# Optimization experiments

Hardware: AMD Instinct MI355X
Metric: run time of the kernel (lower is better)

Reference implementation:

```python
import jax, jax.numpy as jnp
import numpy as np
import math

B, N, C, EV, H = 16, 4096, 256, 64, 8
A_, B_, C_ = 10, 10, 10  # query group sizes a, b, c
TEMP = 0.1


def setup_inputs() -> dict:
    key = jax.random.key(0)
    ks = jax.random.split(key, 24)
    x = jax.random.normal(ks[0], (B, N, C), jnp.float32)
    origin_x = jax.random.normal(ks[1], (B, N, C), jnp.float32)
    evectors = jax.random.normal(ks[2], (B, A_ + B_ + C_, EV), jnp.float32)
    # numv: cumulative node counts; per-graph diff with 3*diff <= N
    diffs = jax.random.randint(ks[3], (B,), 64, N // 3 + 1)
    numv = jnp.concatenate([jnp.zeros((1,), jnp.int32), jnp.cumsum(diffs).astype(jnp.int32)])
    # additive cross mask: valid where position < 3*diff
    pos = jnp.arange(N)
    valid = pos[None, :] < (3 * diffs)[:, None]  # [B, N]
    mask_cross = jnp.where(valid, 0.0, -1e9).astype(jnp.float32)[:, None, :] * jnp.ones((1, A_ + B_ + C_, 1), jnp.float32)
    s = 0.02
    p = lambda k, shp: jax.random.normal(k, shp, jnp.float32) * s
    inp = {
        'x': x, 'origin_x': origin_x, 'evectors': evectors,
        'mask_cross': mask_cross, 'numv': numv,
        'Wq_G': p(ks[4], (C, EV)), 'Wq_D': p(ks[5], (C, EV)), 'Wq_L': p(ks[6], (C, EV)),
        'Wk_G': p(ks[7], (C, C)), 'Wk_D': p(ks[8], (C, C)), 'Wk_L': p(ks[9], (C, C)),
        'Wv_G': p(ks[10], (C, C)), 'bv_G': jnp.zeros((C,), jnp.float32),
        'Wv_D': p(ks[11], (C, C)), 'bv_D': jnp.zeros((C,), jnp.float32),
        'Wv_L': p(ks[12], (C, C)), 'bv_L': jnp.zeros((C,), jnp.float32),
        'Wo': p(ks[13], (C, C)), 'bo': jnp.zeros((C,), jnp.float32),
    }
    return inp


def _forward(x, origin_x, evectors, mask_cross, numv,
             Wq_G, Wq_D, Wq_L, Wk_G, Wk_D, Wk_L,
             Wv_G, bv_G, Wv_D, bv_D, Wv_L, bv_L, Wo, bo):
    dv = C
    dh = dv // H
    nq = A_ + B_ + C_
    # --- query: per-group linear projections on evectors ---
    Q = jnp.concatenate([
        evectors[:, :A_] @ Wq_G.T,
        evectors[:, A_:A_ + B_] @ Wq_D.T,
        evectors[:, A_ + B_:nq] @ Wq_L.T,
    ], axis=1)  # [B, nq, dv]
    # --- ragged K/V construction: group by position vs per-graph diff ---
    diffs = (numv[1:] - numv[:-1]).astype(jnp.int32)  # [B]
    pos = jnp.arange(N)[None, :]  # [1, N]
    d = diffs[:, None]
    g0 = (pos < d).astype(x.dtype)[..., None]
    g1 = ((pos >= d) & (pos < 2 * d)).astype(x.dtype)[..., None]
    g2 = ((pos >= 2 * d) & (pos < 3 * d)).astype(x.dtype)[..., None]
    Kd = g0 * (x @ Wk_G.T) + g1 * (x @ Wk_D.T) + g2 * (x @ Wk_L.T)  # [B, N, dv]
    Vd = (g0 * (origin_x @ Wv_G.T + bv_G)
          + g1 * (origin_x @ Wv_D.T + bv_D)
          + g2 * (origin_x @ Wv_L.T + bv_L))  # [B, N, dv]
    # --- per-head weight decorrelation loss on Q ---
    Qh = Q.reshape(B, nq, H, dh).transpose(2, 0, 1, 3)  # [H, B, nq, dh]
    wd = jnp.asarray(0.0, Q.dtype)
    for lo, sz in ((0, A_), (A_, B_), (A_ + B_, C_)):
        if sz > 1:
            G = Qh[:, :, lo:lo + sz]  # [H, B, sz, dh]
            corr = jnp.einsum('hbik,hbjk->hbij', G, G)
            diff_m = corr - jnp.eye(sz, dtype=Q.dtype)
            fro = jnp.sqrt(jnp.sum(diff_m * diff_m, axis=(-2, -1)))  # [H, B]
            wd = wd + fro.mean(axis=1).sum()
    # --- masked, temperature-scaled multi-head attention ---
    Kh = Kd.reshape(B, N, H, dh)
    Vh = Vd.reshape(B, N, H, dh)
    Qh2 = Q.reshape(B, nq, H, dh)
    scores = jnp.einsum('bqhd,bkhd->bhqk', Qh2, Kh) / (math.sqrt(dv) * TEMP)
    scores = scores + mask_cross[:, None, :, :]
    Aw = jax.nn.softmax(scores, axis=-1)
    out = jnp.einsum('bhqk,bkhd->bqhd', Aw, Vh).reshape(B, nq, dv)
    out = out + jax.nn.relu(out @ Wo.T + bo)
    nrm = jnp.linalg.norm(out, axis=2, keepdims=True)
    out = out / jnp.maximum(nrm, 1e-12)
    return out, wd


def reference(x, origin_x, evectors, mask_cross, numv,
              Wq_G, Wq_D, Wq_L, Wk_G, Wk_D, Wk_L,
              Wv_G, bv_G, Wv_D, bv_D, Wv_L, bv_L, Wo, bo):
    return _forward(x, origin_x, evectors, mask_cross, numv,
                    Wq_G, Wq_D, Wq_L, Wk_G, Wk_D, Wk_L,
                    Wv_G, bv_G, Wv_D, bv_D, Wv_L, bv_L, Wo, bo)
```

## Files before the change

### kernel.cpp

```cpp
#include <hip/hip_runtime.h>
#include <math.h>


typedef __bf16 bf16x8 __attribute__((ext_vector_type(8)));
typedef float  f32x4  __attribute__((ext_vector_type(4)));

namespace {
constexpr int kB   = 16;
constexpr int kN   = 4096;
constexpr int kC   = 256;
constexpr int kEV  = 64;
constexpr int kH   = 8;
constexpr int kDH  = 32;
constexpr int kNQ  = 30;
constexpr int kCH  = 64;
constexpr int kMaxT = 1056;
constexpr int kGrid = 512;
constexpr float kScale = 0.625f;
}

__device__ __forceinline__ unsigned short f32_to_bf16(float f) {
  unsigned int u = __float_as_uint(f);
  unsigned int r = (u + 0x7FFFu + ((u >> 16) & 1u)) >> 16;
  return (unsigned short)r;
}
__device__ __forceinline__ unsigned int pack_bf16(float a, float b) {
  return (unsigned int)f32_to_bf16(a) | ((unsigned int)f32_to_bf16(b) << 16);
}
__device__ __forceinline__ f32x4 splat4(float v) {
  f32x4 r; r[0] = v; r[1] = v; r[2] = v; r[3] = v; return r;
}
__device__ __forceinline__ int swz_f(int row) {
  return ((row & 7) << 2) | (((row >> 3) & 1) << 1);
}

__global__ __launch_bounds__(256) void prep_kernel(
    const float* __restrict__ ev,
    const float* __restrict__ WqG, const float* __restrict__ WqD,
    const float* __restrict__ WqL,
    const float* __restrict__ WkG, const float* __restrict__ WkD,
    const float* __restrict__ WkL,
    const float* __restrict__ WvG, const float* __restrict__ WvD,
    const float* __restrict__ WvL,
    unsigned short* __restrict__ Wb,
    unsigned short* __restrict__ WkT,
    float* __restrict__ Qw, unsigned short* __restrict__ Qb,
    float* __restrict__ wdp)
{
  const int bid = blockIdx.x, tid = threadIdx.x;

  if (bid < 96) {
    const int mat = bid >> 5;
    const float* src = (mat == 0) ? WvG : (mat == 1) ? WvD : WvL;
    const int i0 = (((bid & 31) << 8) + tid) * 8;
    const float4* s4 = (const float4*)(src + i0);
    float4 a = s4[0], b = s4[1];
    uint4 pack = make_uint4(pack_bf16(a.x, a.y), pack_bf16(a.z, a.w),
                            pack_bf16(b.x, b.y), pack_bf16(b.z, b.w));
    *(uint4*)(Wb + (size_t)mat * 65536 + i0) = pack;
    return;
  }

  if (bid < 144) {
    __shared__ float ts[64][65];
    const int t2 = bid - 96;
    const int mat = t2 >> 4, tile = t2 & 15;
    const int r0 = (tile >> 2) * 64, c0 = (tile & 3) * 64;
    const float* src = (mat == 0) ? WkG : (mat == 1) ? WkD : WkL;
#pragma unroll
    for (int it = 0; it < 16; ++it) {
      const int idx = tid + it * 256;
      const int r = idx >> 6, c = idx & 63;
      ts[r][c] = src[(size_t)(r0 + r) * kC + c0 + c];
    }
    __syncthreads();
#pragma unroll
    for (int it = 0; it < 16; ++it) {
      const int idx = tid + it * 256;
      const int r = idx >> 6, c = idx & 63;
      WkT[(size_t)mat * 65536 + (size_t)(c0 + r) * kC + r0 + c] =
          f32_to_bf16(ts[c][r]);
    }
    return;
  }

  if (bid < 656) {
    __shared__ float e[kEV];
    const int idx = bid - 144;
    const int b = idx >> 5, qq = idx & 31;
    if (qq >= kNQ) { Qb[((size_t)(b * 32 + qq)) * kC + tid] = 0; return; }
    if (tid < kEV) e[tid] = ev[((size_t)(b * kNQ + qq)) * kEV + tid];
    __syncthreads();
    const float* W = (qq < 10) ? WqG : (qq < 20) ? WqD : WqL;
    const float4* wr = (const float4*)(W + (size_t)tid * kEV);
    const float4* er = (const float4*)e;
    float s = 0.0f;
#pragma unroll
    for (int j = 0; j < kEV / 4; ++j) {
      float4 w = wr[j], v = er[j];
      s = fmaf(v.x, w.x, s); s = fmaf(v.y, w.y, s);
      s = fmaf(v.z, w.z, s); s = fmaf(v.w, w.w, s);
    }
    Qw[((size_t)(b * kNQ + qq)) * kC + tid] = s;
    Qb[((size_t)(b * 32 + qq)) * kC + tid] = f32_to_bf16(s * kScale);
    return;
  }

  {
    __shared__ float evs[10][64];
    __shared__ float Qblk[10][33];
    __shared__ float sred[256];
    const int w = bid - 656;
    const int b = w / 24, r = w % 24, g = r >> 3, h = r & 7;
    const int lo = g * 10;
    const float* Wqg = (g == 0) ? WqG : (g == 1) ? WqD : WqL;
    for (int i = tid; i < 640; i += 256) {
      const int q = i >> 6, e2 = i & 63;
      evs[q][e2] = ev[((size_t)(b * kNQ + lo + q)) * kEV + e2];
    }
    __syncthreads();
    for (int i = tid; i < 320; i += 256) {
      const int q = i >> 5, kk = i & 31;
      const float* wp = Wqg + (size_t)(h * 32 + kk) * kEV;
      float s = 0.0f;
#pragma unroll
      for (int e4 = 0; e4 < 16; ++e4) {
        float4 ev4 = *(const float4*)&evs[q][e4 * 4];
        float4 w4  = *(const float4*)(wp + e4 * 4);
        s = fmaf(ev4.x, w4.x, s); s = fmaf(ev4.y, w4.y, s);
        s = fmaf(ev4.z, w4.z, s); s = fmaf(ev4.w, w4.w, s);
      }
      Qblk[q][kk] = s;
    }
    __syncthreads();
    float v = 0.0f;
    if (tid < 100) {
      const int i = tid / 10, j = tid % 10;
      float corr = 0.0f;
#pragma unroll
      for (int k = 0; k < kDH; ++k) corr = fmaf(Qblk[i][k], Qblk[j][k], corr);
      const float diff = corr - (i == j ? 1.0f : 0.0f);
      v = diff * diff;
    }
    sred[tid] = v;
    __syncthreads();
    for (int s2 = 128; s2 > 0; s2 >>= 1) {
      if (tid < s2) sred[tid] += sred[tid + s2];
      __syncthreads();
    }
    if (tid == 0) wdp[w] = sqrtf(sred[0]) * (1.0f / 16.0f);
  }
}

__global__ __launch_bounds__(512) void wqk_kernel(
    const unsigned short* __restrict__ Qb,
    const unsigned short* __restrict__ WkT,
    unsigned short* __restrict__ Wqkb)
{
  const int bid = blockIdx.x, tid = threadIdx.x;
  const int b = bid / 3, g = bid % 3;
  const int lane = tid & 63, h = tid >> 6;
  const int lg = lane >> 4, lr = lane & 15;

  const unsigned short* WkT_g = WkT + (size_t)g * 65536;

  bf16x8 aq[2];
#pragma unroll
  for (int mt = 0; mt < 2; ++mt)
    aq[mt] = *reinterpret_cast<const bf16x8*>(
        Qb + (size_t)(b * 32 + mt * 16 + lr) * kC + h * 32 + lg * 8);

  f32x4 acc[2][16];
#pragma unroll
  for (int mt = 0; mt < 2; ++mt)
#pragma unroll
    for (int nt = 0; nt < 16; ++nt) acc[mt][nt] = splat4(0.0f);

#pragma unroll
  for (int nt = 0; nt < 16; ++nt) {
    bf16x8 bw = *reinterpret_cast<const bf16x8*>(
        WkT_g + (size_t)(nt * 16 + lr) * kC + h * 32 + lg * 8);
    acc[0][nt] = __builtin_amdgcn_mfma_f32_16x16x32_bf16(aq[0], bw, acc[0][nt], 0, 0, 0);
    acc[1][nt] = __builtin_amdgcn_mfma_f32_16x16x32_bf16(aq[1], bw, acc[1][nt], 0, 0, 0);
  }

  unsigned short* dst = Wqkb + ((size_t)((b * 3 + g) * 8 + h)) * 32 * kC;
#pragma unroll
  for (int mt = 0; mt < 2; ++mt)
#pragma unroll
    for (int nt = 0; nt < 16; ++nt)
#pragma unroll
      for (int j = 0; j < 4; ++j) {
        const int q = mt * 16 + lg * 4 + j;
        dst[(size_t)q * kC + nt * 16 + lr] = f32_to_bf16(acc[mt][nt][j]);
      }
}

__global__ __launch_bounds__(512, 4) void chunk_kernel(
    const float* __restrict__ x, const float* __restrict__ ox,
    const int* __restrict__ numv,
    const unsigned short* __restrict__ Wb,
    const float* __restrict__ bvG, const float* __restrict__ bvD,
    const float* __restrict__ bvL,
    const unsigned short* __restrict__ Wqkb,
    float* __restrict__ Pl, float* __restrict__ Po)
{
  __shared__ unsigned short Xs[kCH * kC];
  __shared__ unsigned short Ov[kCH * kC];

  const int tid = threadIdx.x;
  const int lane = tid & 63, wv = tid >> 6;
  const int lg = lane >> 4, lr = lane & 15;
  const int wcol0 = wv * 32;
  const int h = wv;

  int nv[17];
#pragma unroll
  for (int i = 0; i < 17; ++i) nv[i] = numv[i];
  int Tall = 0;
#pragma unroll
  for (int bb = 0; bb < kB; ++bb)
    Tall += 3 * ((nv[bb + 1] - nv[bb] + 63) >> 6);

  const int vp = (blockIdx.x & 7) * (kGrid / 8) + (blockIdx.x >> 3);
  const int lo = (vp * Tall) / kGrid;
  const int hi = ((vp + 1) * Tall) / kGrid;

  for (int tt = lo; tt < hi; ++tt) {
    int rem = tt, b = -1, g = 0, ch = 0;
#pragma unroll
    for (int bb = 0; bb < kB; ++bb) {
      const int cb = (nv[bb + 1] - nv[bb] + 63) >> 6;
#pragma unroll
      for (int gg = 0; gg < 3; ++gg) {
        if (b < 0) { if (rem < cb) { b = bb; g = gg; ch = rem; } else rem -= cb; }
      }
    }

    const int d = nv[b + 1] - nv[b];
    const int row0 = g * d + ch * kCH;
    const int nvalid = min(min(kCH, d - ch * kCH), kN - row0);

    const unsigned short* Wv_g = Wb + (size_t)g * 65536;
    const float* bv = (g == 0) ? bvG : (g == 1) ? bvD : bvL;
    const unsigned short* Wqk_h =
        Wqkb + ((size_t)((b * 3 + g) * 8 + h)) * 32 * kC;

    {
      const float* xb = x + (size_t)b * kN * kC;
      const float* ob = ox + (size_t)b * kN * kC;
      float4 xa[8], oa[8];
      int off[4];
#pragma unroll
      for (int i = 0; i < 4; ++i) {
        const int cid = tid + i * 512;
        const int row = cid >> 5, c5 = cid & 31;
        const int rg = min(row0 + row, kN - 1);
        off[i] = rg * kC + c5 * 8;
        const float4* sx = (const float4*)(xb + off[i]);
        xa[2 * i] = sx[0]; xa[2 * i + 1] = sx[1];
      }
#pragma unroll
      for (int i = 0; i < 4; ++i) {
        const float4* so = (const float4*)(ob + off[i]);
        oa[2 * i] = so[0]; oa[2 * i + 1] = so[1];
      }
#pragma unroll
      for (int i = 0; i < 4; ++i) {
        const int cid = tid + i * 512;
        const int row = cid >> 5, c5 = cid & 31;
        const int base = row * kC + ((c5 ^ swz_f(row)) * 8);
        *(uint4*)(Xs + base) = make_uint4(
            pack_bf16(xa[2 * i].x, xa[2 * i].y), pack_bf16(xa[2 * i].z, xa[2 * i].w),
            pack_bf16(xa[2 * i + 1].x, xa[2 * i + 1].y),
            pack_bf16(xa[2 * i + 1].z, xa[2 * i + 1].w));
        *(uint4*)(Ov + base) = make_uint4(
            pack_bf16(oa[2 * i].x, oa[2 * i].y), pack_bf16(oa[2 * i].z, oa[2 * i].w),
            pack_bf16(oa[2 * i + 1].x, oa[2 * i + 1].y),
            pack_bf16(oa[2 * i + 1].z, oa[2 * i + 1].w));
      }
    }
    __syncthreads();

    f32x4 s[4][2];
#pragma unroll
    for (int m = 0; m < 4; ++m)
#pragma unroll
      for (int n = 0; n < 2; ++n) s[m][n] = splat4(0.0f);

#pragma unroll
    for (int kt = 0; kt < 8; ++kt) {
      bf16x8 a[4];
#pragma unroll
      for (int m = 0; m < 4; ++m) {
        const int row = m * 16 + lr;
        const int c16 = (kt * 4 + lg) ^ swz_f(row);
        a[m] = *reinterpret_cast<const bf16x8*>(Xs + row * kC + c16 * 8);
      }
      const int k0 = kt * 32 + lg * 8;
#pragma unroll
      for (int n = 0; n < 2; ++n) {
        bf16x8 bq = *reinterpret_cast<const bf16x8*>(
            Wqk_h + (size_t)(n * 16 + lr) * kC + k0);
#pragma unroll
        for (int m = 0; m < 4; ++m)
          s[m][n] = __builtin_amdgcn_mfma_f32_16x16x32_bf16(a[m], bq, s[m][n], 0, 0, 0);
      }
    }

    unsigned int pp[4][2][2];
    f32x4 lsum[2];
    lsum[0] = splat4(0.0f); lsum[1] = splat4(0.0f);
#pragma unroll
    for (int m = 0; m < 4; ++m)
#pragma unroll
      for (int n = 0; n < 2; ++n) {
        f32x4 pv;
#pragma unroll
        for (int j = 0; j < 4; ++j) {
          const int key = m * 16 + lg * 4 + j;
          pv[j] = (key < nvalid) ? __expf(s[m][n][j]) : 0.0f;
        }
        lsum[n] += pv;
        pp[m][n][0] = pack_bf16(pv[0], pv[1]);
        pp[m][n][1] = pack_bf16(pv[2], pv[3]);
      }
    float ls[2];
#pragma unroll
    for (int n = 0; n < 2; ++n) {
      float v = (lsum[n][0] + lsum[n][1]) + (lsum[n][2] + lsum[n][3]);
      v += __shfl_xor(v, 16);
      v += __shfl_xor(v, 32);
      ls[n] = v;
    }
    if (lg == 0) {
#pragma unroll
      for (int n = 0; n < 2; ++n) {
        const int q = n * 16 + lr;
        if (q < kNQ) Pl[((size_t)tt * kNQ + q) * kH + h] = ls[n];
      }
    }

    f32x4 vacc[4][2];
#pragma unroll
    for (int n = 0; n < 2; ++n) {
      const float bvv = bv[wcol0 + n * 16 + lr];
#pragma unroll
      for (int m = 0; m < 4; ++m) vacc[m][n] = splat4(bvv);
    }
#pragma unroll
    for (int kt = 0; kt < 8; ++kt) {
      bf16x8 a[4];
#pragma unroll
      for (int m = 0; m < 4; ++m) {
        const int row = m * 16 + lr;
        const int c16 = (kt * 4 + lg) ^ swz_f(row);
        a[m] = *reinterpret_cast<const bf16x8*>(Ov + row * kC + c16 * 8);
      }
      const int k0 = kt * 32 + lg * 8;
#pragma unroll
      for (int n = 0; n < 2; ++n) {
        bf16x8 bw = *reinterpret_cast<const bf16x8*>(
            Wv_g + (size_t)(wcol0 + n * 16 + lr) * kC + k0);
#pragma unroll
        for (int m = 0; m < 4; ++m)
          vacc[m][n] = __builtin_amdgcn_mfma_f32_16x16x32_bf16(a[m], bw, vacc[m][n], 0, 0, 0);
      }
    }
    __syncthreads();

    unsigned short* Pw = Xs + wv * 2048;
#pragma unroll
    for (int m = 0; m < 4; ++m)
#pragma unroll
      for (int n = 0; n < 2; ++n) {
        const int q = n * 16 + lr;
        const int ckp = (2 * m + (lg >> 1)) ^ (q & 7);
        unsigned short* pa = Pw + q * kCH + ckp * 8 + (lg & 1) * 4;
        *(unsigned int*)(pa) = pp[m][n][0];
        *(unsigned int*)(pa + 2) = pp[m][n][1];
      }

#pragma unroll
    for (int m = 0; m < 4; ++m)
#pragma unroll
      for (int n = 0; n < 2; ++n) {
        const int col = wcol0 + n * 16 + lr;
        const int r0 = m * 16 + lg * 4;
        unsigned short us[4];
#pragma unroll
        for (int j = 0; j < 4; ++j) us[j] = f32_to_bf16(vacc[m][n][j]);
        const int ck = (r0 >> 3) ^ (col & 7);
        *(uint2*)(Ov + col * kCH + ck * 8 + (r0 & 7)) =
            make_uint2((unsigned int)us[0] | ((unsigned int)us[1] << 16),
                       (unsigned int)us[2] | ((unsigned int)us[3] << 16));
      }

    f32x4 o[2][2];
#pragma unroll
    for (int m = 0; m < 2; ++m)
#pragma unroll
      for (int n = 0; n < 2; ++n) o[m][n] = splat4(0.0f);

#pragma unroll
    for (int ks = 0; ks < 2; ++ks) {
      bf16x8 ap[2];
#pragma unroll
      for (int mq = 0; mq < 2; ++mq) {
        const int q = mq * 16 + lr;
        ap[mq] = *reinterpret_cast<const bf16x8*>(
            Pw + q * kCH + (((ks * 4 + lg) ^ (q & 7))) * 8);
      }
#pragma unroll
      for (int n = 0; n < 2; ++n) {
        const int col = wcol0 + n * 16 + lr;
        bf16x8 bvf = *reinterpret_cast<const bf16x8*>(
            Ov + col * kCH + (((ks * 4 + lg) ^ (col & 7))) * 8);
        o[0][n] = __builtin_amdgcn_mfma_f32_16x16x32_bf16(ap[0], bvf, o[0][n], 0, 0, 0);
        o[1][n] = __builtin_amdgcn_mfma_f32_16x16x32_bf16(ap[1], bvf, o[1][n], 0, 0, 0);
      }
    }

#pragma unroll
    for (int mq = 0; mq < 2; ++mq)
#pragma unroll
      for (int n = 0; n < 2; ++n)
#pragma unroll
        for (int j = 0; j < 4; ++j) {
          const int q = mq * 16 + lg * 4 + j;
          if (q < kNQ)
            Po[(((size_t)tt * kNQ + q) * kH + h) * kDH + n * 16 + lr] = o[mq][n][j];
        }

    if (tt + 1 < hi) __syncthreads();
  }
}

__global__ __launch_bounds__(256) void combine_kernel(
    const float* __restrict__ Pl, const float* __restrict__ Po,
    const int* __restrict__ numv,
    const float* __restrict__ Wo, const float* __restrict__ bo,
    const float* __restrict__ wdp,
    float* __restrict__ out)
{
  const int bq = blockIdx.x;
  const int tid = threadIdx.x;

  if (bq == kB * kNQ) {
    float v = wdp[tid] + ((tid < 128) ? wdp[tid + 256] : 0.0f);
#pragma unroll
    for (int off = 32; off > 0; off >>= 1) v += __shfl_down(v, off);
    __shared__ float red[4];
    if ((tid & 63) == 0) red[tid >> 6] = v;
    __syncthreads();
    if (tid == 0)
      out[(size_t)kB * kNQ * kC] = red[0] + red[1] + red[2] + red[3];
    return;
  }

  const int b = bq / kNQ, q = bq % kNQ;
  const int h = tid >> 5, kk = tid & 31;

  int base = 0, cnt = 0, S = 0;
#pragma unroll
  for (int bb = 0; bb < kB; ++bb) {
    const int c3 = 3 * ((numv[bb + 1] - numv[bb] + 63) >> 6);
    if (bb == b) { base = S; cnt = c3; }
    S += c3;
  }

  float l = 0.0f, oacc = 0.0f;
#pragma unroll 4
  for (int i = 0; i < cnt; ++i) {
    const size_t idx = ((size_t)(base + i) * kNQ + q) * kH + h;
    l += Pl[idx];
    oacc += Po[idx * kDH + kk];
  }
  const float attn = oacc / l;

  __shared__ float row[kC];
  row[tid] = attn;
  __syncthreads();

  const float4* wr = (const float4*)(Wo + (size_t)tid * kC);
  const float4* rr = (const float4*)row;
  float s = 0.0f;
#pragma unroll
  for (int j = 0; j < kC / 4; ++j) {
    float4 w = wr[j], v = rr[j];
    s = fmaf(v.x, w.x, s); s = fmaf(v.y, w.y, s);
    s = fmaf(v.z, w.z, s); s = fmaf(v.w, w.w, s);
  }
  s += bo[tid];
  const float y = attn + fmaxf(s, 0.0f);

  float v = y * y;
#pragma unroll
  for (int off = 32; off > 0; off >>= 1) v += __shfl_down(v, off);
  __shared__ float red[4];
  if ((tid & 63) == 0) red[tid >> 6] = v;
  __syncthreads();
  const float tot = red[0] + red[1] + red[2] + red[3];
  const float nrm = fmaxf(sqrtf(tot), 1e-12f);
  out[(size_t)bq * kC + tid] = y / nrm;
}

extern "C" void kernel_launch(void* const* d_in, const int* in_sizes, int n_in,
                              void* d_out, int out_size, void* d_ws, size_t ws_size,
                              hipStream_t stream) {
  const float* x    = (const float*)d_in[0];
  const float* ox   = (const float*)d_in[1];
  const float* ev   = (const float*)d_in[2];
  const int*   numv = (const int*)d_in[4];
  const float* WqG  = (const float*)d_in[5];
  const float* WqD  = (const float*)d_in[6];
  const float* WqL  = (const float*)d_in[7];
  const float* WkG  = (const float*)d_in[8];
  const float* WkD  = (const float*)d_in[9];
  const float* WkL  = (const float*)d_in[10];
  const float* WvG  = (const float*)d_in[11];
  const float* bvG  = (const float*)d_in[12];
  const float* WvD  = (const float*)d_in[13];
  const float* bvD  = (const float*)d_in[14];
  const float* WvL  = (const float*)d_in[15];
  const float* bvL  = (const float*)d_in[16];
  const float* Wo   = (const float*)d_in[17];
  const float* bo   = (const float*)d_in[18];

  float* out = (float*)d_out;
  char*  ws  = (char*)d_ws;

  size_t off = 0;
  float* Qw = (float*)(ws + off);                   off += 491520;
  unsigned short* Qb   = (unsigned short*)(ws + off); off += 262144;
  unsigned short* Wb   = (unsigned short*)(ws + off); off += 393216;
  unsigned short* WkT  = (unsigned short*)(ws + off); off += 393216;
  unsigned short* Wqkb = (unsigned short*)(ws + off); off += 6291456;
  float* Pl  = (float*)(ws + off);  off += (size_t)kMaxT * kNQ * kH * 4;
  float* Po  = (float*)(ws + off);  off += (size_t)kMaxT * kNQ * kH * kDH * 4;
  float* wdp = (float*)(ws + off);  off += 1536;

  prep_kernel<<<1040, 256, 0, stream>>>(ev, WqG, WqD, WqL,
                                        WkG, WkD, WkL, WvG, WvD, WvL,
                                        Wb, WkT, Qw, Qb, wdp);
  wqk_kernel<<<48, 512, 0, stream>>>(Qb, WkT, Wqkb);
  chunk_kernel<<<kGrid, 512, 0, stream>>>(
      x, ox, numv, Wb, bvG, bvD, bvL, Wqkb, Pl, Po);
  combine_kernel<<<kB * kNQ + 1, 256, 0, stream>>>(Pl, Po, numv, Wo, bo, wdp, out);
}
```

Baseline: 105.2 us.

## Halve attention chunk size, store partial outputs in bf16, double occupancy

Chunk size drops from 64 to 32 keys, which halves LDS and register use per block so the launch bound can ask for 8 blocks per CU instead of 4. The V tile is now stored per wave in LDS. Partial attention outputs are written as bf16 through LDS with vectorized stores, and the combine kernel reads them as bf16. This doubles the number of partial tiles the combine kernel must reduce and lowers the precision of the partial sums.

```diff
diff --git a/kernel.cpp b/kernel.cpp
--- a/kernel.cpp
+++ b/kernel.cpp
@@ -13,8 +13,8 @@
 constexpr int kH   = 8;
 constexpr int kDH  = 32;
 constexpr int kNQ  = 30;
-constexpr int kCH  = 64;
-constexpr int kMaxT = 1056;
+constexpr int kCH  = 32;
+constexpr int kMaxT = 2064;
 constexpr int kGrid = 512;
 constexpr float kScale = 0.625f;
 }
@@ -26,6 +26,9 @@
 }
 __device__ __forceinline__ unsigned int pack_bf16(float a, float b) {
   return (unsigned int)f32_to_bf16(a) | ((unsigned int)f32_to_bf16(b) << 16);
+}
+__device__ __forceinline__ float bf16_to_f32(unsigned short u) {
+  return __uint_as_float((unsigned int)u << 16);
 }
 __device__ __forceinline__ f32x4 splat4(float v) {
   f32x4 r; r[0] = v; r[1] = v; r[2] = v; r[3] = v; return r;
@@ -196,14 +199,14 @@
       }
 }
 
-__global__ __launch_bounds__(512, 4) void chunk_kernel(
+__global__ __launch_bounds__(512, 8) void chunk_kernel(
     const float* __restrict__ x, const float* __restrict__ ox,
     const int* __restrict__ numv,
     const unsigned short* __restrict__ Wb,
     const float* __restrict__ bvG, const float* __restrict__ bvD,
     const float* __restrict__ bvL,
     const unsigned short* __restrict__ Wqkb,
-    float* __restrict__ Pl, float* __restrict__ Po)
+    float* __restrict__ Pl, unsigned short* __restrict__ Po)
 {
   __shared__ unsigned short Xs[kCH * kC];
   __shared__ unsigned short Ov[kCH * kC];
@@ -220,7 +223,7 @@
   int Tall = 0;
 #pragma unroll
   for (int bb = 0; bb < kB; ++bb)
-    Tall += 3 * ((nv[bb + 1] - nv[bb] + 63) >> 6);
+    Tall += 3 * ((nv[bb + 1] - nv[bb] + kCH - 1) / kCH);
 
   const int vp = (blockIdx.x & 7) * (kGrid / 8) + (blockIdx.x >> 3);
   const int lo = (vp * Tall) / kGrid;
@@ -230,7 +233,7 @@
     int rem = tt, b = -1, g = 0, ch = 0;
 #pragma unroll
     for (int bb = 0; bb < kB; ++bb) {
-      const int cb = (nv[bb + 1] - nv[bb] + 63) >> 6;
+      const int cb = (nv[bb + 1] - nv[bb] + kCH - 1) / kCH;
 #pragma unroll
       for (int gg = 0; gg < 3; ++gg) {
         if (b < 0) { if (rem < cb) { b = bb; g = gg; ch = rem; } else rem -= cb; }
@@ -239,7 +242,7 @@
 
     const int d = nv[b + 1] - nv[b];
     const int row0 = g * d + ch * kCH;
-    const int nvalid = min(min(kCH, d - ch * kCH), kN - row0);
+    const int nvalid = min(kCH, d - ch * kCH);
 
     const unsigned short* Wv_g = Wb + (size_t)g * 65536;
     const float* bv = (g == 0) ? bvG : (g == 1) ? bvD : bvL;
@@ -249,26 +252,26 @@
     {
       const float* xb = x + (size_t)b * kN * kC;
       const float* ob = ox + (size_t)b * kN * kC;
-      float4 xa[8], oa[8];
-      int off[4];
-#pragma unroll
-      for (int i = 0; i < 4; ++i) {
-        const int cid = tid + i * 512;
-        const int row = cid >> 5, c5 = cid & 31;
+      float4 xa[4], oa[4];
+      int off[2];
+#pragma unroll
+      for (int i = 0; i < 2; ++i) {
+        const int sid = tid + i * 512;
+        const int row = sid >> 5, c5 = sid & 31;
         const int rg = min(row0 + row, kN - 1);
         off[i] = rg * kC + c5 * 8;
         const float4* sx = (const float4*)(xb + off[i]);
         xa[2 * i] = sx[0]; xa[2 * i + 1] = sx[1];
       }
 #pragma unroll
-      for (int i = 0; i < 4; ++i) {
+      for (int i = 0; i < 2; ++i) {
         const float4* so = (const float4*)(ob + off[i]);
         oa[2 * i] = so[0]; oa[2 * i + 1] = so[1];
       }
 #pragma unroll
-      for (int i = 0; i < 4; ++i) {
-        const int cid = tid + i * 512;
-        const int row = cid >> 5, c5 = cid & 31;
+      for (int i = 0; i < 2; ++i) {
+        const int sid = tid + i * 512;
+        const int row = sid >> 5, c5 = sid & 31;
         const int base = row * kC + ((c5 ^ swz_f(row)) * 8);
         *(uint4*)(Xs + base) = make_uint4(
             pack_bf16(xa[2 * i].x, xa[2 * i].y), pack_bf16(xa[2 * i].z, xa[2 * i].w),
@@ -282,17 +285,17 @@
     }
     __syncthreads();
 
-    f32x4 s[4][2];
-#pragma unroll
-    for (int m = 0; m < 4; ++m)
+    f32x4 s[2][2];
+#pragma unroll
+    for (int m = 0; m < 2; ++m)
 #pragma unroll
       for (int n = 0; n < 2; ++n) s[m][n] = splat4(0.0f);
 
 #pragma unroll
     for (int kt = 0; kt < 8; ++kt) {
-      bf16x8 a[4];
-#pragma unroll
-      for (int m = 0; m < 4; ++m) {
+      bf16x8 a[2];
+#pragma unroll
+      for (int m = 0; m < 2; ++m) {
         const int row = m * 16 + lr;
         const int c16 = (kt * 4 + lg) ^ swz_f(row);
         a[m] = *reinterpret_cast<const bf16x8*>(Xs + row * kC + c16 * 8);
@@ -303,16 +306,16 @@
         bf16x8 bq = *reinterpret_cast<const bf16x8*>(
             Wqk_h + (size_t)(n * 16 + lr) * kC + k0);
 #pragma unroll
-        for (int m = 0; m < 4; ++m)
+        for (int m = 0; m < 2; ++m)
           s[m][n] = __builtin_amdgcn_mfma_f32_16x16x32_bf16(a[m], bq, s[m][n], 0, 0, 0);
       }
     }
 
-    unsigned int pp[4][2][2];
+    unsigned int pp[2][2][2];
     f32x4 lsum[2];
     lsum[0] = splat4(0.0f); lsum[1] = splat4(0.0f);
 #pragma unroll
-    for (int m = 0; m < 4; ++m)
+    for (int m = 0; m < 2; ++m)
 #pragma unroll
       for (int n = 0; n < 2; ++n) {
         f32x4 pv;
@@ -341,18 +344,18 @@
       }
     }
 
-    f32x4 vacc[4][2];
+    f32x4 vacc[2][2];
 #pragma unroll
     for (int n = 0; n < 2; ++n) {
       const float bvv = bv[wcol0 + n * 16 + lr];
 #pragma unroll
-      for (int m = 0; m < 4; ++m) vacc[m][n] = splat4(bvv);
+      for (int m = 0; m < 2; ++m) vacc[m][n] = splat4(bvv);
     }
 #pragma unroll
     for (int kt = 0; kt < 8; ++kt) {
-      bf16x8 a[4];
-#pragma unroll
-      for (int m = 0; m < 4; ++m) {
+      bf16x8 a[2];
+#pragma unroll
+      for (int m = 0; m < 2; ++m) {
         const int row = m * 16 + lr;
         const int c16 = (kt * 4 + lg) ^ swz_f(row);
         a[m] = *reinterpret_cast<const bf16x8*>(Ov + row * kC + c16 * 8);
@@ -363,37 +366,37 @@
         bf16x8 bw = *reinterpret_cast<const bf16x8*>(
             Wv_g + (size_t)(wcol0 + n * 16 + lr) * kC + k0);
 #pragma unroll
-        for (int m = 0; m < 4; ++m)
+        for (int m = 0; m < 2; ++m)
           vacc[m][n] = __builtin_amdgcn_mfma_f32_16x16x32_bf16(a[m], bw, vacc[m][n], 0, 0, 0);
       }
     }
     __syncthreads();
 
-    unsigned short* Pw = Xs + wv * 2048;
-#pragma unroll
-    for (int m = 0; m < 4; ++m)
+    unsigned short* Pw = Xs + wv * 1024;
+#pragma unroll
+    for (int m = 0; m < 2; ++m)
 #pragma unroll
       for (int n = 0; n < 2; ++n) {
         const int q = n * 16 + lr;
-        const int ckp = (2 * m + (lg >> 1)) ^ (q & 7);
-        unsigned short* pa = Pw + q * kCH + ckp * 8 + (lg & 1) * 4;
+        const int ck = (2 * m + (lg >> 1)) ^ (q & 3);
+        unsigned short* pa = Pw + q * kCH + ck * 8 + (lg & 1) * 4;
         *(unsigned int*)(pa) = pp[m][n][0];
         *(unsigned int*)(pa + 2) = pp[m][n][1];
       }
 
-#pragma unroll
-    for (int m = 0; m < 4; ++m)
-#pragma unroll
-      for (int n = 0; n < 2; ++n) {
-        const int col = wcol0 + n * 16 + lr;
-        const int r0 = m * 16 + lg * 4;
-        unsigned short us[4];
-#pragma unroll
-        for (int j = 0; j < 4; ++j) us[j] = f32_to_bf16(vacc[m][n][j]);
-        const int ck = (r0 >> 3) ^ (col & 7);
-        *(uint2*)(Ov + col * kCH + ck * 8 + (r0 & 7)) =
-            make_uint2((unsigned int)us[0] | ((unsigned int)us[1] << 16),
-                       (unsigned int)us[2] | ((unsigned int)us[3] << 16));
+    unsigned short* Vw = Ov + wv * 1024;
+#pragma unroll
+    for (int m = 0; m < 2; ++m)
+#pragma unroll
+      for (int n = 0; n < 2; ++n) {
+        const int cl = n * 16 + lr;
+        const int k0r = m * 16 + lg * 4;
+        const int ck = (2 * m + (lg >> 1)) ^ (cl & 3);
+        *(unsigned int*)(Vw + cl * kCH + ck * 8 + (lg & 1) * 4) =
+            pack_bf16(vacc[m][n][0], vacc[m][n][1]);
+        *(unsigned int*)(Vw + cl * kCH + ck * 8 + (lg & 1) * 4 + 2) =
+            pack_bf16(vacc[m][n][2], vacc[m][n][3]);
+        (void)k0r;
       }
 
     f32x4 o[2][2];
@@ -402,20 +405,19 @@
 #pragma unroll
       for (int n = 0; n < 2; ++n) o[m][n] = splat4(0.0f);
 
-#pragma unroll
-    for (int ks = 0; ks < 2; ++ks) {
+    {
       bf16x8 ap[2];
 #pragma unroll
       for (int mq = 0; mq < 2; ++mq) {
         const int q = mq * 16 + lr;
         ap[mq] = *reinterpret_cast<const bf16x8*>(
-            Pw + q * kCH + (((ks * 4 + lg) ^ (q & 7))) * 8);
-      }
-#pragma unroll
-      for (int n = 0; n < 2; ++n) {
-        const int col = wcol0 + n * 16 + lr;
+            Pw + q * kCH + ((lg ^ (q & 3))) * 8);
+      }
+#pragma unroll
+      for (int n = 0; n < 2; ++n) {
+        const int cl = n * 16 + lr;
         bf16x8 bvf = *reinterpret_cast<const bf16x8*>(
-            Ov + col * kCH + (((ks * 4 + lg) ^ (col & 7))) * 8);
+            Vw + cl * kCH + ((lg ^ (cl & 3))) * 8);
         o[0][n] = __builtin_amdgcn_mfma_f32_16x16x32_bf16(ap[0], bvf, o[0][n], 0, 0, 0);
         o[1][n] = __builtin_amdgcn_mfma_f32_16x16x32_bf16(ap[1], bvf, o[1][n], 0, 0, 0);
       }
@@ -428,16 +430,24 @@
 #pragma unroll
         for (int j = 0; j < 4; ++j) {
           const int q = mq * 16 + lg * 4 + j;
-          if (q < kNQ)
-            Po[(((size_t)tt * kNQ + q) * kH + h) * kDH + n * 16 + lr] = o[mq][n][j];
+          Pw[q * kDH + n * 16 + lr] = f32_to_bf16(o[mq][n][j]);
         }
+    {
+      unsigned short* pdst = Po + (((size_t)tt * kNQ) * kH + h) * kDH;
+#pragma unroll 2
+      for (int idx = lane; idx < kNQ * 4; idx += 64) {
+        const int q = idx >> 2, c = idx & 3;
+        uint4 v4 = *(const uint4*)(Pw + q * kDH + c * 8);
+        *(uint4*)(pdst + (size_t)q * kH * kDH + c * 8) = v4;
+      }
+    }
 
     if (tt + 1 < hi) __syncthreads();
   }
 }
 
 __global__ __launch_bounds__(256) void combine_kernel(
-    const float* __restrict__ Pl, const float* __restrict__ Po,
+    const float* __restrict__ Pl, const unsigned short* __restrict__ Po,
     const int* __restrict__ numv,
     const float* __restrict__ Wo, const float* __restrict__ bo,
     const float* __restrict__ wdp,
@@ -464,7 +474,7 @@
   int base = 0, cnt = 0, S = 0;
 #pragma unroll
   for (int bb = 0; bb < kB; ++bb) {
-    const int c3 = 3 * ((numv[bb + 1] - numv[bb] + 63) >> 6);
+    const int c3 = 3 * ((numv[bb + 1] - numv[bb] + kCH - 1) / kCH);
     if (bb == b) { base = S; cnt = c3; }
     S += c3;
   }
@@ -474,7 +484,7 @@
   for (int i = 0; i < cnt; ++i) {
     const size_t idx = ((size_t)(base + i) * kNQ + q) * kH + h;
     l += Pl[idx];
-    oacc += Po[idx * kDH + kk];
+    oacc += bf16_to_f32(Po[idx * kDH + kk]);
   }
   const float attn = oacc / l;
 
@@ -536,9 +546,10 @@
   unsigned short* Wb   = (unsigned short*)(ws + off); off += 393216;
   unsigned short* WkT  = (unsigned short*)(ws + off); off += 393216;
   unsigned short* Wqkb = (unsigned short*)(ws + off); off += 6291456;
-  float* Pl  = (float*)(ws + off);  off += (size_t)kMaxT * kNQ * kH * 4;
-  float* Po  = (float*)(ws + off);  off += (size_t)kMaxT * kNQ * kH * kDH * 4;
-  float* wdp = (float*)(ws + off);  off += 1536;
+  float* Pl = (float*)(ws + off);           off += (size_t)kMaxT * kNQ * kH * 4;
+  unsigned short* Po = (unsigned short*)(ws + off);
+  off += (size_t)kMaxT * kNQ * kH * kDH * 2;
+  float* wdp = (float*)(ws + off);          off += 1536;
 
   prep_kernel<<<1040, 256, 0, stream>>>(ev, WqG, WqD, WqL,
                                         WkG, WkD, WkL, WvG, WvD, WvL,
```

New measurement: 153.7 us. 46.1% more time.

## Prefetch next chunk's inputs into registers and store partial outputs as bf16

Applied to the files above, without the earlier changes.

The chunk kernel now loads the next chunk's x/origin_x rows into registers right after the LDS barrier, so the global loads overlap the current chunk's MFMA work. The grid is halved to 256 and the occupancy hint drops to 2 blocks per CU to make room for the extra live registers. Partial attention outputs are staged in LDS and written as bf16 in a head-major layout with coalesced 16-byte stores, which halves Po traffic for the combine kernel at some precision cost. Plain __syncthreads are replaced by a barrier that waits only on LDS counters.

```diff
diff --git a/kernel.cpp b/kernel.cpp
--- a/kernel.cpp
+++ b/kernel.cpp
@@ -15,9 +15,15 @@
 constexpr int kNQ  = 30;
 constexpr int kCH  = 64;
 constexpr int kMaxT = 1056;
-constexpr int kGrid = 512;
+constexpr int kGrid = 256;
 constexpr float kScale = 0.625f;
 }
+
+#define BAR_LDS() do {                                        \
+    asm volatile("s_waitcnt lgkmcnt(0)" ::: "memory");        \
+    __builtin_amdgcn_s_barrier();                             \
+    __builtin_amdgcn_sched_barrier(0);                        \
+  } while (0)
 
 __device__ __forceinline__ unsigned short f32_to_bf16(float f) {
   unsigned int u = __float_as_uint(f);
@@ -26,6 +32,9 @@
 }
 __device__ __forceinline__ unsigned int pack_bf16(float a, float b) {
   return (unsigned int)f32_to_bf16(a) | ((unsigned int)f32_to_bf16(b) << 16);
+}
+__device__ __forceinline__ float bf16_to_f32(unsigned short u) {
+  return __uint_as_float((unsigned int)u << 16);
 }
 __device__ __forceinline__ f32x4 splat4(float v) {
   f32x4 r; r[0] = v; r[1] = v; r[2] = v; r[3] = v; return r;
@@ -196,14 +205,14 @@
       }
 }
 
-__global__ __launch_bounds__(512, 4) void chunk_kernel(
+__global__ __launch_bounds__(512, 2) void chunk_kernel(
     const float* __restrict__ x, const float* __restrict__ ox,
     const int* __restrict__ numv,
     const unsigned short* __restrict__ Wb,
     const float* __restrict__ bvG, const float* __restrict__ bvD,
     const float* __restrict__ bvL,
     const unsigned short* __restrict__ Wqkb,
-    float* __restrict__ Pl, float* __restrict__ Po)
+    float* __restrict__ Pl, unsigned short* __restrict__ Po)
 {
   __shared__ unsigned short Xs[kCH * kC];
   __shared__ unsigned short Ov[kCH * kC];
@@ -220,23 +229,50 @@
   int Tall = 0;
 #pragma unroll
   for (int bb = 0; bb < kB; ++bb)
-    Tall += 3 * ((nv[bb + 1] - nv[bb] + 63) >> 6);
+    Tall += 3 * ((nv[bb + 1] - nv[bb] + kCH - 1) / kCH);
 
   const int vp = (blockIdx.x & 7) * (kGrid / 8) + (blockIdx.x >> 3);
   const int lo = (vp * Tall) / kGrid;
   const int hi = ((vp + 1) * Tall) / kGrid;
-
-  for (int tt = lo; tt < hi; ++tt) {
-    int rem = tt, b = -1, g = 0, ch = 0;
+  if (lo >= hi) return;
+
+  auto decode = [&](int tt, int& b, int& g, int& ch) {
+    int rem = tt; b = -1; g = 0; ch = 0;
 #pragma unroll
     for (int bb = 0; bb < kB; ++bb) {
-      const int cb = (nv[bb + 1] - nv[bb] + 63) >> 6;
+      const int cb = (nv[bb + 1] - nv[bb] + kCH - 1) / kCH;
 #pragma unroll
       for (int gg = 0; gg < 3; ++gg) {
         if (b < 0) { if (rem < cb) { b = bb; g = gg; ch = rem; } else rem -= cb; }
       }
     }
-
+  };
+
+  float4 xa[8], oa[8];
+  auto issue = [&](int b, int g, int ch) {
+    const int d = nv[b + 1] - nv[b];
+    const int row0 = g * d + ch * kCH;
+    const float* xb = x + (size_t)b * kN * kC;
+    const float* ob = ox + (size_t)b * kN * kC;
+#pragma unroll
+    for (int i = 0; i < 4; ++i) {
+      const int cid = tid + i * 512;
+      const int row = cid >> 5, c5 = cid & 31;
+      const int rg = min(row0 + row, kN - 1);
+      const size_t off = (size_t)rg * kC + c5 * 8;
+      const float4* sx = (const float4*)(xb + off);
+      xa[2 * i] = sx[0]; xa[2 * i + 1] = sx[1];
+      const float4* so = (const float4*)(ob + off);
+      oa[2 * i] = so[0]; oa[2 * i + 1] = so[1];
+    }
+  };
+
+  int pb, pg, pch;
+  decode(lo, pb, pg, pch);
+  issue(pb, pg, pch);
+
+  for (int tt = lo; tt < hi; ++tt) {
+    const int b = pb, g = pg, ch = pch;
     const int d = nv[b + 1] - nv[b];
     const int row0 = g * d + ch * kCH;
     const int nvalid = min(min(kCH, d - ch * kCH), kN - row0);
@@ -246,41 +282,23 @@
     const unsigned short* Wqk_h =
         Wqkb + ((size_t)((b * 3 + g) * 8 + h)) * 32 * kC;
 
-    {
-      const float* xb = x + (size_t)b * kN * kC;
-      const float* ob = ox + (size_t)b * kN * kC;
-      float4 xa[8], oa[8];
-      int off[4];
-#pragma unroll
-      for (int i = 0; i < 4; ++i) {
-        const int cid = tid + i * 512;
-        const int row = cid >> 5, c5 = cid & 31;
-        const int rg = min(row0 + row, kN - 1);
-        off[i] = rg * kC + c5 * 8;
-        const float4* sx = (const float4*)(xb + off[i]);
-        xa[2 * i] = sx[0]; xa[2 * i + 1] = sx[1];
-      }
-#pragma unroll
-      for (int i = 0; i < 4; ++i) {
-        const float4* so = (const float4*)(ob + off[i]);
-        oa[2 * i] = so[0]; oa[2 * i + 1] = so[1];
-      }
-#pragma unroll
-      for (int i = 0; i < 4; ++i) {
-        const int cid = tid + i * 512;
-        const int row = cid >> 5, c5 = cid & 31;
-        const int base = row * kC + ((c5 ^ swz_f(row)) * 8);
-        *(uint4*)(Xs + base) = make_uint4(
-            pack_bf16(xa[2 * i].x, xa[2 * i].y), pack_bf16(xa[2 * i].z, xa[2 * i].w),
-            pack_bf16(xa[2 * i + 1].x, xa[2 * i + 1].y),
-            pack_bf16(xa[2 * i + 1].z, xa[2 * i + 1].w));
-        *(uint4*)(Ov + base) = make_uint4(
-            pack_bf16(oa[2 * i].x, oa[2 * i].y), pack_bf16(oa[2 * i].z, oa[2 * i].w),
-            pack_bf16(oa[2 * i + 1].x, oa[2 * i + 1].y),
-            pack_bf16(oa[2 * i + 1].z, oa[2 * i + 1].w));
-      }
-    }
-    __syncthreads();
+#pragma unroll
+    for (int i = 0; i < 4; ++i) {
+      const int cid = tid + i * 512;
+      const int row = cid >> 5, c5 = cid & 31;
+      const int base = row * kC + ((c5 ^ swz_f(row)) * 8);
+      *(uint4*)(Xs + base) = make_uint4(
+          pack_bf16(xa[2 * i].x, xa[2 * i].y), pack_bf16(xa[2 * i].z, xa[2 * i].w),
+          pack_bf16(xa[2 * i + 1].x, xa[2 * i + 1].y),
+          pack_bf16(xa[2 * i + 1].z, xa[2 * i + 1].w));
+      *(uint4*)(Ov + base) = make_uint4(
+          pack_bf16(oa[2 * i].x, oa[2 * i].y), pack_bf16(oa[2 * i].z, oa[2 * i].w),
+          pack_bf16(oa[2 * i + 1].x, oa[2 * i + 1].y),
+          pack_bf16(oa[2 * i + 1].z, oa[2 * i + 1].w));
+    }
+    BAR_LDS();
+
+    if (tt + 1 < hi) { decode(tt + 1, pb, pg, pch); issue(pb, pg, pch); }
 
     f32x4 s[4][2];
 #pragma unroll
@@ -367,7 +385,7 @@
           vacc[m][n] = __builtin_amdgcn_mfma_f32_16x16x32_bf16(a[m], bw, vacc[m][n], 0, 0, 0);
       }
     }
-    __syncthreads();
+    BAR_LDS();
 
     unsigned short* Pw = Xs + wv * 2048;
 #pragma unroll
@@ -387,13 +405,10 @@
       for (int n = 0; n < 2; ++n) {
         const int col = wcol0 + n * 16 + lr;
         const int r0 = m * 16 + lg * 4;
-        unsigned short us[4];
-#pragma unroll
-        for (int j = 0; j < 4; ++j) us[j] = f32_to_bf16(vacc[m][n][j]);
         const int ck = (r0 >> 3) ^ (col & 7);
         *(uint2*)(Ov + col * kCH + ck * 8 + (r0 & 7)) =
-            make_uint2((unsigned int)us[0] | ((unsigned int)us[1] << 16),
-                       (unsigned int)us[2] | ((unsigned int)us[3] << 16));
+            make_uint2(pack_bf16(vacc[m][n][0], vacc[m][n][1]),
+                       pack_bf16(vacc[m][n][2], vacc[m][n][3]));
       }
 
     f32x4 o[2][2];
@@ -428,16 +443,22 @@
 #pragma unroll
         for (int j = 0; j < 4; ++j) {
           const int q = mq * 16 + lg * 4 + j;
-          if (q < kNQ)
-            Po[(((size_t)tt * kNQ + q) * kH + h) * kDH + n * 16 + lr] = o[mq][n][j];
+          Pw[q * kDH + n * 16 + lr] = f32_to_bf16(o[mq][n][j]);
         }
-
-    if (tt + 1 < hi) __syncthreads();
+    {
+      unsigned short* pdst = Po + ((size_t)tt * kH + h) * (kNQ * kDH);
+      if (lane < 120) {
+        uint4 v4 = *(const uint4*)(Pw + lane * 8);
+        *(uint4*)(pdst + lane * 8) = v4;
+      }
+    }
+
+    if (tt + 1 < hi) BAR_LDS();
   }
 }
 
 __global__ __launch_bounds__(256) void combine_kernel(
-    const float* __restrict__ Pl, const float* __restrict__ Po,
+    const float* __restrict__ Pl, const unsigned short* __restrict__ Po,
     const int* __restrict__ numv,
     const float* __restrict__ Wo, const float* __restrict__ bo,
     const float* __restrict__ wdp,
@@ -464,7 +485,7 @@
   int base = 0, cnt = 0, S = 0;
 #pragma unroll
   for (int bb = 0; bb < kB; ++bb) {
-    const int c3 = 3 * ((numv[bb + 1] - numv[bb] + 63) >> 6);
+    const int c3 = 3 * ((numv[bb + 1] - numv[bb] + kCH - 1) / kCH);
     if (bb == b) { base = S; cnt = c3; }
     S += c3;
   }
@@ -472,9 +493,9 @@
   float l = 0.0f, oacc = 0.0f;
 #pragma unroll 4
   for (int i = 0; i < cnt; ++i) {
-    const size_t idx = ((size_t)(base + i) * kNQ + q) * kH + h;
-    l += Pl[idx];
-    oacc += Po[idx * kDH + kk];
+    const int t = base + i;
+    l += Pl[((size_t)t * kNQ + q) * kH + h];
+    oacc += bf16_to_f32(Po[((size_t)t * kH + h) * (kNQ * kDH) + q * kDH + kk]);
   }
   const float attn = oacc / l;
 
@@ -536,9 +557,10 @@
   unsigned short* Wb   = (unsigned short*)(ws + off); off += 393216;
   unsigned short* WkT  = (unsigned short*)(ws + off); off += 393216;
   unsigned short* Wqkb = (unsigned short*)(ws + off); off += 6291456;
-  float* Pl  = (float*)(ws + off);  off += (size_t)kMaxT * kNQ * kH * 4;
-  float* Po  = (float*)(ws + off);  off += (size_t)kMaxT * kNQ * kH * kDH * 4;
-  float* wdp = (float*)(ws + off);  off += 1536;
+  float* Pl = (float*)(ws + off);           off += (size_t)kMaxT * kNQ * kH * 4;
+  unsigned short* Po = (unsigned short*)(ws + off);
+  off += (size_t)kMaxT * kH * kNQ * kDH * 2;
+  float* wdp = (float*)(ws + off);          off += 1536;
 
   prep_kernel<<<1040, 256, 0, stream>>>(ev, WqG, WqD, WqL,
                                         WkG, WkD, WkL, WvG, WvD, WvL,
```

Result: faster. 95.76 us (-9.0%).
